# Kernel tuning notes

Measured on AMD Instinct MI355X. Metric: run time of the kernel, lower is better.

Reference implementation:

```python
import jax, jax.numpy as jnp
import numpy as np

G = 2   # FlipGroup order
H = 16  # num_heads
TEMPERATURE = 1.0


def _shared_w(A, B):
    # Z2 regular-representation equivariant linear: block-circulant weight
    # W = [[A, B], [B, A]], shape (dim, dim)
    return jnp.concatenate([
        jnp.concatenate([A, B], axis=1),
        jnp.concatenate([B, A], axis=1),
    ], axis=0)


def setup_inputs() -> dict:
    key = jax.random.key(0)
    ks = jax.random.split(key, 9)
    d = 1024
    dh = d // G
    inp = {"x": jax.random.normal(ks[0], (4, 1024, d), jnp.float32)}
    for i, n in enumerate(["wqA", "wqB", "wkA", "wkB", "wvA", "wvB", "wpA", "wpB"]):
        inp[n] = jax.random.normal(ks[i + 1], (dh, dh), jnp.float32) * 0.02
    return inp


def reference(x, wqA, wqB, wkA, wkB, wvA, wvB, wpA, wpB):
    B, N, C = x.shape
    hd = C // G // H            # per-group-channel head dim
    scale = hd ** -0.5

    q = x @ _shared_w(wqA, wqB).T
    k = x @ _shared_w(wkA, wkB).T
    v = x @ _shared_w(wvA, wvB).T

    def split(t):
        # (B,N,C) -> (B,H,G,N,hd): per-head features split into G group channels
        return t.reshape(B, N, H, G, hd).transpose(0, 2, 3, 1, 4)

    q, k, v = split(q), split(k), split(v)

    # per-channel attention: independent softmax per (head, group-channel)
    attn = jax.nn.softmax(
        jnp.einsum('bhgnd,bhgmd->bhgnm', q, k) * (scale / TEMPERATURE), axis=-1)
    o = jnp.einsum('bhgnm,bhgmd->bhgnd', attn, v)

    o = o.transpose(0, 3, 1, 2, 4).reshape(B, N, C)
    return o @ _shared_w(wpA, wpB).T
```

## Files before the change

### kernel.cpp

```cpp
#include <hip/hip_runtime.h>


typedef unsigned short ushort_t;
typedef __attribute__((ext_vector_type(4))) unsigned short ushort4_t;
typedef __attribute__((ext_vector_type(8))) unsigned short ushort8;
typedef __attribute__((ext_vector_type(8))) __bf16 bf16x8;
typedef __attribute__((ext_vector_type(4))) float f32x4;
typedef __attribute__((ext_vector_type(4))) unsigned int uint4_t;

#define GPTR(p) ((const __attribute__((address_space(1))) void*)(p))
#define LPTR(p) ((__attribute__((address_space(3))) void*)(p))

static __device__ __forceinline__ unsigned short f2b(float f) {
  unsigned int u = __builtin_bit_cast(unsigned int, f);
  unsigned int r = u + 0x7fffu + ((u >> 16) & 1u);
  return (unsigned short)(r >> 16);
}
static __device__ __forceinline__ float b2f(ushort_t h) {
  unsigned int u = ((unsigned int)h) << 16;
  return __builtin_bit_cast(float, u);
}
static __device__ __forceinline__ unsigned int pack_rtna(float a, float b) {
  const unsigned int ua = (__builtin_bit_cast(unsigned int, a) + 0x8000u) >> 16;
  const unsigned int ub = (__builtin_bit_cast(unsigned int, b) + 0x8000u) & 0xFFFF0000u;
  return ub | ua;
}

__global__ __launch_bounds__(256) void prep_k(
    const float* __restrict__ x,
    const float* __restrict__ wqA, const float* __restrict__ wqB,
    const float* __restrict__ wkA, const float* __restrict__ wkB,
    const float* __restrict__ wvA, const float* __restrict__ wvB,
    const float* __restrict__ wpA, const float* __restrict__ wpB,
    ushort_t* __restrict__ xsd, ushort_t* __restrict__ Wsd, float sclq) {
  const int bid = blockIdx.x;
  if (bid < 1024) {
    const int u = bid * 256 + threadIdx.x;
    const int m = u >> 6;
    const int k8 = (u & 63) * 8;
    const float* p1 = x + (size_t)m * 1024 + k8;
    const float* p2 = p1 + 512;
    const f32x4 a0 = *(const f32x4*)p1,  a1 = *(const f32x4*)(p1 + 4);
    const f32x4 b0 = *(const f32x4*)p2,  b1 = *(const f32x4*)(p2 + 4);
    ushort8 vs, vd;
#pragma unroll
    for (int e = 0; e < 4; ++e) {
      vs[e] = f2b(a0[e] + b0[e]); vs[e + 4] = f2b(a1[e] + b1[e]);
      vd[e] = f2b(a0[e] - b0[e]); vd[e + 4] = f2b(a1[e] - b1[e]);
    }
    *(ushort8*)&xsd[(size_t)m * 1024 + k8] = vs;
    *(ushort8*)&xsd[(size_t)m * 1024 + 512 + k8] = vd;
  } else {
    const int u = (bid - 1024) * 256 + threadIdx.x;
    const int hm = u >> 15;
    const int rem = u & 32767;
    const int r = rem >> 6;
    const int c8 = (rem & 63) * 8;
    const int proj = hm >> 1, isD = hm & 1;
    const float* A; const float* B;
    if (proj == 0)      { A = wqA; B = wqB; }
    else if (proj == 1) { A = wkA; B = wkB; }
    else if (proj == 2) { A = wvA; B = wvB; }
    else                { A = wpA; B = wpB; }
    const float scl = 0.5f * (proj == 0 ? sclq : 1.0f);
    const f32x4 a0 = *(const f32x4*)(A + (size_t)r * 512 + c8);
    const f32x4 a1 = *(const f32x4*)(A + (size_t)r * 512 + c8 + 4);
    const f32x4 b0 = *(const f32x4*)(B + (size_t)r * 512 + c8);
    const f32x4 b1 = *(const f32x4*)(B + (size_t)r * 512 + c8 + 4);
    ushort8 v;
#pragma unroll
    for (int e = 0; e < 4; ++e) {
      v[e]     = f2b(isD ? (a0[e] - b0[e]) * scl : (a0[e] + b0[e]) * scl);
      v[e + 4] = f2b(isD ? (a1[e] - b1[e]) * scl : (a1[e] + b1[e]) * scl);
    }
    *(ushort8*)&Wsd[(size_t)(proj * 1024 + isD * 512 + r) * 512 + c8] = v;
  }
}

__global__ __launch_bounds__(256, 3) void gemm_sd_qkv(const ushort_t* __restrict__ xsd,
                                                      const ushort_t* __restrict__ Wsd,
                                                      ushort_t* __restrict__ Qb,
                                                      ushort_t* __restrict__ Kb,
                                                      ushort_t* __restrict__ Vtb) {
  __shared__ ushort_t sh[24576];

  const int t = threadIdx.x;
  const int wid = t >> 6, lane = t & 63;
  const int wm = wid >> 1, half = wid & 1;
  const int lr = lane & 15, lg = lane >> 4;

  const int bid = blockIdx.x;
  const int c = bid & 7, j = bid >> 3;
  const int mt = c * 4 + (j & 3);
  const int nzt = j >> 2;
  const int z = nzt >> 3;
  const int n0 = (nzt & 7) * 64;
  const int m0 = mt * 128;

  f32x4 acc[4][4];
  const f32x4 fz = {0.f, 0.f, 0.f, 0.f};
#pragma unroll
  for (int mf = 0; mf < 4; ++mf)
#pragma unroll
    for (int nf = 0; nf < 4; ++nf) acc[mf][nf] = fz;

#define ISSUE(kt_, s_)                                                                   \
  {                                                                                      \
    ushort_t* base_ = sh + (s_) * 12288;                                                 \
    const int k0_ = (kt_) * 32;                                                          \
    _Pragma("unroll") for (int rnd = 0; rnd < 2; ++rnd) {                                \
      const int ch = rnd * 256 + t;                                                      \
      const int row = ch >> 2, cs = ch & 3;                                              \
      const int gcol = k0_ + ((cs ^ ((row >> 1) & 3)) << 3);                             \
      __builtin_amdgcn_global_load_lds(GPTR(xsd + (size_t)(m0 + row) * 1024 + gcol),     \
                                       LPTR(base_ + (size_t)ch * 8), 16, 0, 0);          \
      __builtin_amdgcn_global_load_lds(GPTR(xsd + (size_t)(m0 + row) * 1024 + 512 + gcol),\
                                       LPTR(base_ + 4096 + (size_t)ch * 8), 16, 0, 0);   \
    }                                                                                    \
    {                                                                                    \
      const int row = t >> 2, cs = t & 3;                                                \
      const int gcol = k0_ + ((cs ^ ((row >> 1) & 3)) << 3);                             \
      __builtin_amdgcn_global_load_lds(                                                  \
          GPTR(Wsd + (size_t)(z * 1024 + n0 + row) * 512 + gcol),                        \
          LPTR(sh + (s_) * 12288 + 8192 + (size_t)t * 8), 16, 0, 0);                     \
      __builtin_amdgcn_global_load_lds(                                                  \
          GPTR(Wsd + (size_t)(z * 1024 + 512 + n0 + row) * 512 + gcol),                  \
          LPTR(sh + (s_) * 12288 + 10240 + (size_t)t * 8), 16, 0, 0);                    \
    }                                                                                    \
  }

  ISSUE(0, 0)
  for (int kt = 0; kt < 16; ++kt) {
    const int s = kt & 1;
    asm volatile("" ::: "memory");
    __builtin_amdgcn_s_barrier();
    asm volatile("" ::: "memory");
    if (kt < 15) {
      ISSUE(kt + 1, s ^ 1)
      asm volatile("s_waitcnt vmcnt(6)" ::: "memory");
    } else {
      asm volatile("s_waitcnt vmcnt(0)" ::: "memory");
    }
    __builtin_amdgcn_sched_barrier(0);
    __builtin_amdgcn_s_barrier();
    asm volatile("" ::: "memory");

    const ushort_t* base = sh + s * 12288;
    const ushort_t* Asl = base + half * 4096;
    const ushort_t* Bsl = base + 8192 + half * 2048;
    bf16x8 a[4], b[4];
#pragma unroll
    for (int mf = 0; mf < 4; ++mf) {
      const int row = wm * 64 + mf * 16 + lr;
      a[mf] = *(const bf16x8*)&Asl[row * 32 + ((lg ^ ((row >> 1) & 3)) << 3)];
    }
#pragma unroll
    for (int nf = 0; nf < 4; ++nf) {
      const int row = nf * 16 + lr;
      b[nf] = *(const bf16x8*)&Bsl[row * 32 + ((lg ^ ((row >> 1) & 3)) << 3)];
    }
    __builtin_amdgcn_s_setprio(1);
#pragma unroll
    for (int mf = 0; mf < 4; ++mf)
#pragma unroll
      for (int nf = 0; nf < 4; ++nf)
        acc[mf][nf] = __builtin_amdgcn_mfma_f32_16x16x32_bf16(a[mf], b[nf], acc[mf][nf], 0, 0, 0);
    __builtin_amdgcn_s_setprio(0);
  }
#undef ISSUE

  __syncthreads();
  const int PAD = (z < 2) ? 72 : 73;
  ushort_t* tus = sh;
  ushort_t* tvd = sh + 128 * PAD;
  {
    ushort_t* dst = half ? tvd : tus;
#pragma unroll
    for (int mf = 0; mf < 4; ++mf)
#pragma unroll
      for (int nf = 0; nf < 4; ++nf)
#pragma unroll
        for (int rr = 0; rr < 4; ++rr) {
          const int row = wm * 64 + mf * 16 + lg * 4 + rr;
          const int col = nf * 16 + lr;
          dst[row * PAD + col] = f2b(acc[mf][nf][rr]);
        }
  }
  __syncthreads();

  if (z < 2) {
    ushort_t* C = (z == 0) ? Qb : Kb;
#pragma unroll
    for (int it = 0; it < 4; ++it) {
      const int idx = it * 256 + t;
      const int row = idx >> 3;
      const int c8 = (idx & 7) * 8;
      const ushort8 u8 = *(const ushort8*)&tus[row * 72 + c8];
      const ushort8 v8 = *(const ushort8*)&tvd[row * 72 + c8];
      ushort8 y1, y2;
#pragma unroll
      for (int e = 0; e < 8; ++e) {
        const float us = b2f(u8[e]), vd = b2f(v8[e]);
        y1[e] = f2b(us + vd);
        y2[e] = f2b(us - vd);
      }
      *(ushort8*)&C[(size_t)(m0 + row) * 1024 + n0 + c8] = y1;
      *(ushort8*)&C[(size_t)(m0 + row) * 1024 + 512 + n0 + c8] = y2;
    }
  } else {
    const int bidx = m0 >> 10, tok0 = m0 & 1023;
#pragma unroll
    for (int it = 0; it < 4; ++it) {
      const int idx = it * 256 + t;
      const int cr = idx >> 4;
      const int mc = (idx & 15) * 8;
      float y1v[8], y2v[8];
#pragma unroll
      for (int e = 0; e < 8; ++e) {
        const float us = b2f(tus[(mc + e) * 73 + cr]);
        const float vd = b2f(tvd[(mc + e) * 73 + cr]);
        y1v[e] = us + vd;
        y2v[e] = us - vd;
      }
      const int k6 = mc & 63;
      const int base = (k6 & 0x20) | ((k6 & 8) << 1) | ((k6 & 0x10) >> 2);
      const size_t rb1 = (size_t)bidx * 1024 * 1024 + (size_t)(n0 + cr) * 1024 +
                         tok0 + (mc & ~63) + base;
      const size_t rb2 = (size_t)bidx * 1024 * 1024 + (size_t)(512 + n0 + cr) * 1024 +
                         tok0 + (mc & ~63) + base;
      ushort4_t lo1, hi1, lo2, hi2;
#pragma unroll
      for (int e = 0; e < 4; ++e) {
        lo1[e] = f2b(y1v[e]); hi1[e] = f2b(y1v[e + 4]);
        lo2[e] = f2b(y2v[e]); hi2[e] = f2b(y2v[e + 4]);
      }
      *(ushort4_t*)&Vtb[rb1] = lo1;  *(ushort4_t*)&Vtb[rb1 + 8] = hi1;
      *(ushort4_t*)&Vtb[rb2] = lo2;  *(ushort4_t*)&Vtb[rb2 + 8] = hi2;
    }
  }
}

__global__ __launch_bounds__(512, 4) void attn_k(const ushort_t* __restrict__ Q,
                                                 const ushort_t* __restrict__ K,
                                                 const ushort_t* __restrict__ Vt,
                                                 ushort_t* __restrict__ Osd) {
  __shared__ ushort_t shmem[32768];
  ushort_t* KsL = shmem;
  ushort_t* VsL = shmem + 16384;
  float* obuf = (float*)shmem;

  const int t = threadIdx.x;
  const int w = t >> 6, lane = t & 63;
  const int hw = w >> 2;
  const int lr = lane & 15, lg = lane >> 4, lk8 = lg * 8;
  const int rkey = (lr >> 1) & 3;
  const int pkey = lr & 7;

  const int nlin = blockIdx.x;
  const int c = nlin & 7, j = nlin >> 3;
  const int p = c * 8 + (j >> 3);
  const int qb = j & 7;
  const int hp = p & 15, b = p >> 4;

  const size_t bbase = (size_t)b * 1024 * 1024;
  const size_t headc = (size_t)hp * 32 + hw * 512;
  const int q0 = qb * 128 + (w & 3) * 32;
  const f32x4 fzero = {0.f, 0.f, 0.f, 0.f};

  bf16x8 bq[2];
#pragma unroll
  for (int i = 0; i < 2; ++i)
    bq[i] = *(const bf16x8*)&Q[bbase + (size_t)(q0 + i * 16 + lr) * 1024 + headc + lk8];

  f32x4 oacc[2][2];
  float tq[2] = {0.f, 0.f};
#pragma unroll
  for (int i = 0; i < 2; ++i)
#pragma unroll
    for (int jj = 0; jj < 2; ++jj) oacc[i][jj] = fzero;

#define ISSUE_KV(kt_, s_)                                                                \
  {                                                                                      \
    ushort_t* Kd_ = KsL + (s_) * 4096;                                                   \
    ushort_t* Vd_ = VsL + (s_) * 4096;                                                   \
    const int hl = t >> 8, rem = t & 255;                                                \
    const size_t hc_ = (size_t)hp * 32 + hl * 512;                                       \
    const int krow = rem >> 2, kc = rem & 3;                                             \
    __builtin_amdgcn_global_load_lds(                                                    \
        GPTR(K + bbase + (size_t)((kt_) * 64 + krow) * 1024 + hc_ +                      \
             ((kc ^ ((krow >> 1) & 3)) << 3)),                                           \
        LPTR(Kd_ + (size_t)t * 8), 16, 0, 0);                                            \
    const int vrow = rem >> 3, vc = rem & 7;                                             \
    __builtin_amdgcn_global_load_lds(                                                    \
        GPTR(Vt + bbase + (size_t)(hc_ + vrow) * 1024 + (kt_) * 64 +                     \
             ((vc ^ (vrow & 7)) << 3)),                                                  \
        LPTR(Vd_ + (size_t)t * 8), 16, 0, 0);                                            \
  }

  ISSUE_KV(0, 0) ISSUE_KV(1, 1) ISSUE_KV(2, 2)
  for (int kt = 0; kt < 16; ++kt) {
    const int s = kt & 3;
    asm volatile("" ::: "memory");
    __builtin_amdgcn_s_barrier();
    asm volatile("" ::: "memory");
    if (kt < 13) {
      ISSUE_KV(kt + 3, (kt + 3) & 3)
      asm volatile("s_waitcnt vmcnt(6)" ::: "memory");
    } else if (kt == 13) {
      asm volatile("s_waitcnt vmcnt(4)" ::: "memory");
    } else if (kt == 14) {
      asm volatile("s_waitcnt vmcnt(2)" ::: "memory");
    } else {
      asm volatile("s_waitcnt vmcnt(0)" ::: "memory");
    }
    __builtin_amdgcn_sched_barrier(0);
    __builtin_amdgcn_s_barrier();
    asm volatile("" ::: "memory");

    const ushort_t* Ksb = KsL + s * 4096 + hw * 2048;
    const ushort_t* Vsb = VsL + s * 4096 + hw * 2048;

    bf16x8 ak[4];
#pragma unroll
    for (int kf = 0; kf < 4; ++kf)
      ak[kf] = *(const bf16x8*)&Ksb[(kf * 16 + lr) * 32 + ((lg ^ rkey) << 3)];

    bf16x8 ap[2][2];
#pragma unroll
    for (int i = 0; i < 2; ++i) {
      f32x4 s4[4];
      __builtin_amdgcn_s_setprio(1);
#pragma unroll
      for (int kf = 0; kf < 4; ++kf)
        s4[kf] = __builtin_amdgcn_mfma_f32_16x16x32_bf16(ak[kf], bq[i], fzero, 0, 0, 0);
      __builtin_amdgcn_s_setprio(0);
#pragma unroll
      for (int ks = 0; ks < 2; ++ks) {
        const float p0 = __builtin_amdgcn_exp2f(s4[2 * ks][0]);
        const float p1 = __builtin_amdgcn_exp2f(s4[2 * ks][1]);
        const float p2 = __builtin_amdgcn_exp2f(s4[2 * ks][2]);
        const float p3 = __builtin_amdgcn_exp2f(s4[2 * ks][3]);
        const float p4 = __builtin_amdgcn_exp2f(s4[2 * ks + 1][0]);
        const float p5 = __builtin_amdgcn_exp2f(s4[2 * ks + 1][1]);
        const float p6 = __builtin_amdgcn_exp2f(s4[2 * ks + 1][2]);
        const float p7 = __builtin_amdgcn_exp2f(s4[2 * ks + 1][3]);
        tq[i] += ((p0 + p1) + (p2 + p3)) + ((p4 + p5) + (p6 + p7));
        uint4_t u;
        u[0] = pack_rtna(p0, p1);
        u[1] = pack_rtna(p2, p3);
        u[2] = pack_rtna(p4, p5);
        u[3] = pack_rtna(p6, p7);
        ap[i][ks] = __builtin_bit_cast(bf16x8, u);
      }
    }

#pragma unroll
    for (int ks = 0; ks < 2; ++ks) {
      bf16x8 bv0 = *(const bf16x8*)&Vsb[(0 * 16 + lr) * 64 + ((ks * 32 + lk8) ^ (pkey << 3))];
      bf16x8 bv1 = *(const bf16x8*)&Vsb[(1 * 16 + lr) * 64 + ((ks * 32 + lk8) ^ (pkey << 3))];
      __builtin_amdgcn_s_setprio(1);
#pragma unroll
      for (int i = 0; i < 2; ++i) {
        oacc[i][0] = __builtin_amdgcn_mfma_f32_16x16x32_bf16(ap[i][ks], bv0, oacc[i][0], 0, 0, 0);
        oacc[i][1] = __builtin_amdgcn_mfma_f32_16x16x32_bf16(ap[i][ks], bv1, oacc[i][1], 0, 0, 0);
      }
      __builtin_amdgcn_s_setprio(0);
    }
  }
#undef ISSUE_KV

#pragma unroll
  for (int i = 0; i < 2; ++i) {
    tq[i] += __shfl_xor(tq[i], 16, 64);
    tq[i] += __shfl_xor(tq[i], 32, 64);
  }

  __syncthreads();
#pragma unroll
  for (int i = 0; i < 2; ++i) {
    float inv[4];
#pragma unroll
    for (int r = 0; r < 4; ++r)
      inv[r] = 1.0f / __shfl(tq[i], lg * 4 + r, 64);
#pragma unroll
    for (int jj = 0; jj < 2; ++jj)
#pragma unroll
      for (int r = 0; r < 4; ++r) {
        const int row = (w & 3) * 32 + i * 16 + lg * 4 + r;
        obuf[hw * 4224 + row * 33 + jj * 16 + lr] = oacc[i][jj][r] * inv[r];
      }
  }
  __syncthreads();

  {
    const int row = t >> 2;
    const int c8 = (t & 3) * 8;
    ushort8 vs, vd;
#pragma unroll
    for (int e = 0; e < 8; ++e) {
      const float o0 = obuf[0 * 4224 + row * 33 + c8 + e];
      const float o1 = obuf[1 * 4224 + row * 33 + c8 + e];
      vs[e] = f2b(o0 + o1);
      vd[e] = f2b(o0 - o1);
    }
    const size_t rowg = bbase + (size_t)(qb * 128 + row) * 1024;
    *(ushort8*)&Osd[rowg + hp * 32 + c8] = vs;
    *(ushort8*)&Osd[rowg + 512 + hp * 32 + c8] = vd;
  }
}

__global__ __launch_bounds__(256, 4) void gemm_out_sd(const ushort_t* __restrict__ Osd,
                                                      const ushort_t* __restrict__ Wsd,
                                                      float* __restrict__ out) {
  __shared__ ushort_t sh[24576];

  const int t = threadIdx.x;
  const int w = t >> 6, lane = t & 63;
  const int wm = w >> 1, half = w & 1;
  const int lr = lane & 15, lg = lane >> 4;

  const int bid = blockIdx.x;
  const int c = bid & 7, j = bid >> 3;
  const int mt = c * 8 + (j & 7);
  const int st = j >> 3;
  const int m0 = mt * 64, n0s = st * 64;

  f32x4 acc[2][4];
  const f32x4 fz = {0.f, 0.f, 0.f, 0.f};
#pragma unroll
  for (int mf = 0; mf < 2; ++mf)
#pragma unroll
    for (int nf = 0; nf < 4; ++nf) acc[mf][nf] = fz;

#define ISSUE_O(kt_, s_)                                                                 \
  {                                                                                      \
    ushort_t* base_ = sh + (s_) * 8192;                                                  \
    const int k0_ = (kt_) * 32;                                                          \
    const int row = t >> 2, kc = t & 3;                                                  \
    const int gcol = k0_ + ((kc ^ ((row >> 1) & 3)) << 3);                               \
    __builtin_amdgcn_global_load_lds(GPTR(Osd + (size_t)(m0 + row) * 1024 + gcol),       \
                                     LPTR(base_ + (size_t)t * 8), 16, 0, 0);             \
    __builtin_amdgcn_global_load_lds(GPTR(Osd + (size_t)(m0 + row) * 1024 + 512 + gcol), \
                                     LPTR(base_ + 2048 + (size_t)t * 8), 16, 0, 0);      \
    __builtin_amdgcn_global_load_lds(                                                    \
        GPTR(Wsd + (size_t)(3072 + n0s + row) * 512 + gcol),                             \
        LPTR(base_ + 4096 + (size_t)t * 8), 16, 0, 0);                                   \
    __builtin_amdgcn_global_load_lds(                                                    \
        GPTR(Wsd + (size_t)(3072 + 512 + n0s + row) * 512 + gcol),                       \
        LPTR(base_ + 6144 + (size_t)t * 8), 16, 0, 0);                                   \
  }

  ISSUE_O(0, 0) ISSUE_O(1, 1)
  int s = 0;
  for (int kt = 0; kt < 16; ++kt) {
    asm volatile("" ::: "memory");
    __builtin_amdgcn_s_barrier();
    asm volatile("" ::: "memory");
    if (kt < 14) {
      const int s2 = (s >= 1) ? s - 1 : 2;
      ISSUE_O(kt + 2, s2)
      asm volatile("s_waitcnt vmcnt(8)" ::: "memory");
    } else if (kt == 14) {
      asm volatile("s_waitcnt vmcnt(4)" ::: "memory");
    } else {
      asm volatile("s_waitcnt vmcnt(0)" ::: "memory");
    }
    __builtin_amdgcn_sched_barrier(0);
    __builtin_amdgcn_s_barrier();
    asm volatile("" ::: "memory");

    const ushort_t* base = sh + s * 8192;
    const ushort_t* Asl = base + half * 2048;
    const ushort_t* Bsl = base + 4096 + half * 2048;
    bf16x8 a[2], b[4];
#pragma unroll
    for (int mf = 0; mf < 2; ++mf) {
      const int row = wm * 32 + mf * 16 + lr;
      a[mf] = *(const bf16x8*)&Asl[row * 32 + ((lg ^ ((row >> 1) & 3)) << 3)];
    }
#pragma unroll
    for (int nf = 0; nf < 4; ++nf) {
      const int row = nf * 16 + lr;
      b[nf] = *(const bf16x8*)&Bsl[row * 32 + ((lg ^ ((row >> 1) & 3)) << 3)];
    }
    __builtin_amdgcn_s_setprio(1);
#pragma unroll
    for (int mf = 0; mf < 2; ++mf)
#pragma unroll
      for (int nf = 0; nf < 4; ++nf)
        acc[mf][nf] = __builtin_amdgcn_mfma_f32_16x16x32_bf16(a[mf], b[nf], acc[mf][nf], 0, 0, 0);
    __builtin_amdgcn_s_setprio(0);
    s = (s == 2) ? 0 : s + 1;
  }
#undef ISSUE_O

  __syncthreads();
  float* vdbuf = (float*)sh;
  if (half == 1) {
#pragma unroll
    for (int mf = 0; mf < 2; ++mf)
#pragma unroll
      for (int nf = 0; nf < 4; ++nf)
#pragma unroll
        for (int rr = 0; rr < 4; ++rr) {
          const int row = wm * 32 + mf * 16 + lg * 4 + rr;
          const int col = nf * 16 + lr;
          vdbuf[row * 66 + col] = acc[mf][nf][rr];
        }
  }
  __syncthreads();
  if (half == 0) {
#pragma unroll
    for (int mf = 0; mf < 2; ++mf)
#pragma unroll
      for (int nf = 0; nf < 4; ++nf)
#pragma unroll
        for (int rr = 0; rr < 4; ++rr) {
          const int row = wm * 32 + mf * 16 + lg * 4 + rr;
          const int col = nf * 16 + lr;
          const float us = acc[mf][nf][rr];
          const float vd = vdbuf[row * 66 + col];
          out[(size_t)(m0 + row) * 1024 + n0s + col] = us + vd;
          out[(size_t)(m0 + row) * 1024 + 512 + n0s + col] = us - vd;
        }
  }
}

extern "C" void kernel_launch(void* const* d_in, const int* in_sizes, int n_in,
                              void* d_out, int out_size, void* d_ws, size_t ws_size,
                              hipStream_t stream) {
  const float* x   = (const float*)d_in[0];
  const float* wqA = (const float*)d_in[1];
  const float* wqB = (const float*)d_in[2];
  const float* wkA = (const float*)d_in[3];
  const float* wkB = (const float*)d_in[4];
  const float* wvA = (const float*)d_in[5];
  const float* wvB = (const float*)d_in[6];
  const float* wpA = (const float*)d_in[7];
  const float* wpB = (const float*)d_in[8];
  float* out = (float*)d_out;

  const size_t NE = (size_t)4096 * 1024;
  ushort_t* Qb   = (ushort_t*)d_ws;
  ushort_t* Kb   = Qb + NE;
  ushort_t* Vtb  = Kb + NE;
  ushort_t* xsd  = Vtb + NE;
  ushort_t* Wsd  = xsd + NE;
  ushort_t* Osd  = xsd;

  const float SCL = 0.17677669529663687f * 1.4426950408889634f;

  prep_k<<<2048, 256, 0, stream>>>(x, wqA, wqB, wkA, wkB, wvA, wvB, wpA, wpB,
                                   xsd, Wsd, SCL);
  gemm_sd_qkv<<<768, 256, 0, stream>>>(xsd, Wsd, Qb, Kb, Vtb);
  attn_k<<<512, 512, 0, stream>>>(Qb, Kb, Vtb, Osd);
  gemm_out_sd<<<512, 256, 0, stream>>>(Osd, Wsd, out);

  (void)in_sizes; (void)n_in; (void)out_size; (void)ws_size;
}
```

Measured before the change: 80.63 us.

## Widen QKV GEMM tile to 128 columns with 512 threads and 4-stage pipeline

The QKV GEMM now uses 512-thread blocks covering a 128x128 output tile (per sum/diff half), halving the grid. The two-stage double buffer is replaced by a four-stage LDS ring with loads issued three steps ahead. The MFMA work is split into two phases with staged X and W loads placed between them. This aims to improve reuse of the x tile and hide global load latency, at the cost of 128 KB of LDS per block, which limits occupancy, and more barriers per k-step.

```diff
diff --git a/kernel.cpp b/kernel.cpp
--- a/kernel.cpp
+++ b/kernel.cpp
@@ -77,25 +77,28 @@
   }
 }
 
-__global__ __launch_bounds__(256, 3) void gemm_sd_qkv(const ushort_t* __restrict__ xsd,
+__global__ __launch_bounds__(512, 2) void gemm_sd_qkv(const ushort_t* __restrict__ xsd,
                                                       const ushort_t* __restrict__ Wsd,
                                                       ushort_t* __restrict__ Qb,
                                                       ushort_t* __restrict__ Kb,
                                                       ushort_t* __restrict__ Vtb) {
-  __shared__ ushort_t sh[24576];
+  __shared__ ushort_t sh[65536];
 
   const int t = threadIdx.x;
   const int wid = t >> 6, lane = t & 63;
-  const int wm = wid >> 1, half = wid & 1;
+  const int wm = wid >> 2, sp = (wid >> 1) & 1, half = wid & 1;
   const int lr = lane & 15, lg = lane >> 4;
 
   const int bid = blockIdx.x;
   const int c = bid & 7, j = bid >> 3;
   const int mt = c * 4 + (j & 3);
-  const int nzt = j >> 2;
-  const int z = nzt >> 3;
-  const int n0 = (nzt & 7) * 64;
+  const int nz = j >> 2;
+  const int z = nz >> 2;
+  const int n0sp = (nz & 3) * 128;
   const int m0 = mt * 128;
+
+  const int srow = t >> 2, scs = t & 3;
+  const int sswz = (scs ^ ((srow >> 1) & 3)) << 3;
 
   f32x4 acc[4][4];
   const f32x4 fz = {0.f, 0.f, 0.f, 0.f};
@@ -104,73 +107,101 @@
 #pragma unroll
     for (int nf = 0; nf < 4; ++nf) acc[mf][nf] = fz;
 
-#define ISSUE(kt_, s_)                                                                   \
+#define STAGE_X(kt_, s_)                                                                 \
   {                                                                                      \
-    ushort_t* base_ = sh + (s_) * 12288;                                                 \
-    const int k0_ = (kt_) * 32;                                                          \
-    _Pragma("unroll") for (int rnd = 0; rnd < 2; ++rnd) {                                \
-      const int ch = rnd * 256 + t;                                                      \
-      const int row = ch >> 2, cs = ch & 3;                                              \
-      const int gcol = k0_ + ((cs ^ ((row >> 1) & 3)) << 3);                             \
-      __builtin_amdgcn_global_load_lds(GPTR(xsd + (size_t)(m0 + row) * 1024 + gcol),     \
-                                       LPTR(base_ + (size_t)ch * 8), 16, 0, 0);          \
-      __builtin_amdgcn_global_load_lds(GPTR(xsd + (size_t)(m0 + row) * 1024 + 512 + gcol),\
-                                       LPTR(base_ + 4096 + (size_t)ch * 8), 16, 0, 0);   \
-    }                                                                                    \
-    {                                                                                    \
-      const int row = t >> 2, cs = t & 3;                                                \
-      const int gcol = k0_ + ((cs ^ ((row >> 1) & 3)) << 3);                             \
-      __builtin_amdgcn_global_load_lds(                                                  \
-          GPTR(Wsd + (size_t)(z * 1024 + n0 + row) * 512 + gcol),                        \
-          LPTR(sh + (s_) * 12288 + 8192 + (size_t)t * 8), 16, 0, 0);                     \
-      __builtin_amdgcn_global_load_lds(                                                  \
-          GPTR(Wsd + (size_t)(z * 1024 + 512 + n0 + row) * 512 + gcol),                  \
-          LPTR(sh + (s_) * 12288 + 10240 + (size_t)t * 8), 16, 0, 0);                    \
-    }                                                                                    \
-  }
-
-  ISSUE(0, 0)
+    ushort_t* b_ = sh + (s_) * 16384;                                                    \
+    const int gcol = (kt_) * 32 + sswz;                                                  \
+    __builtin_amdgcn_global_load_lds(GPTR(xsd + (size_t)(m0 + srow) * 1024 + gcol),      \
+                                     LPTR(b_ + (size_t)t * 8), 16, 0, 0);                \
+    __builtin_amdgcn_global_load_lds(GPTR(xsd + (size_t)(m0 + srow) * 1024 + 512 + gcol),\
+                                     LPTR(b_ + 4096 + (size_t)t * 8), 16, 0, 0);         \
+  }
+#define STAGE_W(kt_, s_)                                                                 \
+  {                                                                                      \
+    ushort_t* b_ = sh + (s_) * 16384;                                                    \
+    const int gcol = (kt_) * 32 + sswz;                                                  \
+    __builtin_amdgcn_global_load_lds(                                                    \
+        GPTR(Wsd + (size_t)(z * 1024 + n0sp + srow) * 512 + gcol),                       \
+        LPTR(b_ + 8192 + (size_t)t * 8), 16, 0, 0);                                      \
+    __builtin_amdgcn_global_load_lds(                                                    \
+        GPTR(Wsd + (size_t)(z * 1024 + 512 + n0sp + srow) * 512 + gcol),                 \
+        LPTR(b_ + 12288 + (size_t)t * 8), 16, 0, 0);                                     \
+  }
+
+  STAGE_X(0, 0) STAGE_W(0, 0)
+  STAGE_X(1, 1) STAGE_W(1, 1)
+  STAGE_X(2, 2) STAGE_W(2, 2)
+  asm volatile("s_waitcnt vmcnt(8)" ::: "memory");
+  __builtin_amdgcn_sched_barrier(0);
+  __builtin_amdgcn_s_barrier();
+  asm volatile("" ::: "memory");
+
   for (int kt = 0; kt < 16; ++kt) {
-    const int s = kt & 1;
-    asm volatile("" ::: "memory");
-    __builtin_amdgcn_s_barrier();
-    asm volatile("" ::: "memory");
-    if (kt < 15) {
-      ISSUE(kt + 1, s ^ 1)
-      asm volatile("s_waitcnt vmcnt(6)" ::: "memory");
-    } else {
+    const int s = kt & 3;
+    const ushort_t* base = sh + s * 16384;
+    const ushort_t* Asl = base + half * 4096;
+    const ushort_t* Bsl = base + 8192 + half * 4096;
+
+    bf16x8 a0, a1, b[4];
+    {
+      const int r0 = wm * 64 + 0 * 16 + lr;
+      const int r1 = wm * 64 + 1 * 16 + lr;
+      a0 = *(const bf16x8*)&Asl[r0 * 32 + ((lg ^ ((r0 >> 1) & 3)) << 3)];
+      a1 = *(const bf16x8*)&Asl[r1 * 32 + ((lg ^ ((r1 >> 1) & 3)) << 3)];
+#pragma unroll
+      for (int nf = 0; nf < 4; ++nf) {
+        const int rb = sp * 64 + nf * 16 + lr;
+        b[nf] = *(const bf16x8*)&Bsl[rb * 32 + ((lg ^ ((rb >> 1) & 3)) << 3)];
+      }
+    }
+    if (kt <= 12) STAGE_X(kt + 3, (kt + 3) & 3)
+    __builtin_amdgcn_s_barrier();
+    asm volatile("s_waitcnt lgkmcnt(0)" ::: "memory");
+    __builtin_amdgcn_sched_barrier(0);
+    __builtin_amdgcn_s_setprio(1);
+#pragma unroll
+    for (int nf = 0; nf < 4; ++nf) {
+      acc[0][nf] = __builtin_amdgcn_mfma_f32_16x16x32_bf16(a0, b[nf], acc[0][nf], 0, 0, 0);
+      acc[1][nf] = __builtin_amdgcn_mfma_f32_16x16x32_bf16(a1, b[nf], acc[1][nf], 0, 0, 0);
+    }
+    __builtin_amdgcn_s_setprio(0);
+    __builtin_amdgcn_s_barrier();
+    asm volatile("" ::: "memory");
+
+    bf16x8 a2, a3;
+    {
+      const int r2 = wm * 64 + 2 * 16 + lr;
+      const int r3 = wm * 64 + 3 * 16 + lr;
+      a2 = *(const bf16x8*)&Asl[r2 * 32 + ((lg ^ ((r2 >> 1) & 3)) << 3)];
+      a3 = *(const bf16x8*)&Asl[r3 * 32 + ((lg ^ ((r3 >> 1) & 3)) << 3)];
+    }
+    if (kt <= 12) STAGE_W(kt + 3, (kt + 3) & 3)
+    if (kt <= 12) {
+      asm volatile("s_waitcnt vmcnt(8)" ::: "memory");
+    } else if (kt == 13) {
+      asm volatile("s_waitcnt vmcnt(4)" ::: "memory");
+    } else if (kt == 14) {
       asm volatile("s_waitcnt vmcnt(0)" ::: "memory");
     }
     __builtin_amdgcn_sched_barrier(0);
     __builtin_amdgcn_s_barrier();
-    asm volatile("" ::: "memory");
-
-    const ushort_t* base = sh + s * 12288;
-    const ushort_t* Asl = base + half * 4096;
-    const ushort_t* Bsl = base + 8192 + half * 2048;
-    bf16x8 a[4], b[4];
-#pragma unroll
-    for (int mf = 0; mf < 4; ++mf) {
-      const int row = wm * 64 + mf * 16 + lr;
-      a[mf] = *(const bf16x8*)&Asl[row * 32 + ((lg ^ ((row >> 1) & 3)) << 3)];
-    }
+    asm volatile("s_waitcnt lgkmcnt(0)" ::: "memory");
+    __builtin_amdgcn_sched_barrier(0);
+    __builtin_amdgcn_s_setprio(1);
 #pragma unroll
     for (int nf = 0; nf < 4; ++nf) {
-      const int row = nf * 16 + lr;
-      b[nf] = *(const bf16x8*)&Bsl[row * 32 + ((lg ^ ((row >> 1) & 3)) << 3)];
-    }
-    __builtin_amdgcn_s_setprio(1);
-#pragma unroll
-    for (int mf = 0; mf < 4; ++mf)
-#pragma unroll
-      for (int nf = 0; nf < 4; ++nf)
-        acc[mf][nf] = __builtin_amdgcn_mfma_f32_16x16x32_bf16(a[mf], b[nf], acc[mf][nf], 0, 0, 0);
+      acc[2][nf] = __builtin_amdgcn_mfma_f32_16x16x32_bf16(a2, b[nf], acc[2][nf], 0, 0, 0);
+      acc[3][nf] = __builtin_amdgcn_mfma_f32_16x16x32_bf16(a3, b[nf], acc[3][nf], 0, 0, 0);
+    }
     __builtin_amdgcn_s_setprio(0);
-  }
-#undef ISSUE
+    __builtin_amdgcn_s_barrier();
+    asm volatile("" ::: "memory");
+  }
+#undef STAGE_X
+#undef STAGE_W
 
   __syncthreads();
-  const int PAD = (z < 2) ? 72 : 73;
+  const int PAD = (z < 2) ? 136 : 137;
   ushort_t* tus = sh;
   ushort_t* tvd = sh + 128 * PAD;
   {
@@ -182,7 +213,7 @@
 #pragma unroll
         for (int rr = 0; rr < 4; ++rr) {
           const int row = wm * 64 + mf * 16 + lg * 4 + rr;
-          const int col = nf * 16 + lr;
+          const int col = sp * 64 + nf * 16 + lr;
           dst[row * PAD + col] = f2b(acc[mf][nf][rr]);
         }
   }
@@ -192,11 +223,11 @@
     ushort_t* C = (z == 0) ? Qb : Kb;
 #pragma unroll
     for (int it = 0; it < 4; ++it) {
-      const int idx = it * 256 + t;
-      const int row = idx >> 3;
-      const int c8 = (idx & 7) * 8;
-      const ushort8 u8 = *(const ushort8*)&tus[row * 72 + c8];
-      const ushort8 v8 = *(const ushort8*)&tvd[row * 72 + c8];
+      const int idx = it * 512 + t;
+      const int row = idx >> 4;
+      const int c8 = (idx & 15) * 8;
+      const ushort8 u8 = *(const ushort8*)&tus[row * 136 + c8];
+      const ushort8 v8 = *(const ushort8*)&tvd[row * 136 + c8];
       ushort8 y1, y2;
 #pragma unroll
       for (int e = 0; e < 8; ++e) {
@@ -204,29 +235,29 @@
         y1[e] = f2b(us + vd);
         y2[e] = f2b(us - vd);
       }
-      *(ushort8*)&C[(size_t)(m0 + row) * 1024 + n0 + c8] = y1;
-      *(ushort8*)&C[(size_t)(m0 + row) * 1024 + 512 + n0 + c8] = y2;
+      *(ushort8*)&C[(size_t)(m0 + row) * 1024 + n0sp + c8] = y1;
+      *(ushort8*)&C[(size_t)(m0 + row) * 1024 + 512 + n0sp + c8] = y2;
     }
   } else {
     const int bidx = m0 >> 10, tok0 = m0 & 1023;
 #pragma unroll
     for (int it = 0; it < 4; ++it) {
-      const int idx = it * 256 + t;
+      const int idx = it * 512 + t;
       const int cr = idx >> 4;
       const int mc = (idx & 15) * 8;
       float y1v[8], y2v[8];
 #pragma unroll
       for (int e = 0; e < 8; ++e) {
-        const float us = b2f(tus[(mc + e) * 73 + cr]);
-        const float vd = b2f(tvd[(mc + e) * 73 + cr]);
+        const float us = b2f(tus[(mc + e) * 137 + cr]);
+        const float vd = b2f(tvd[(mc + e) * 137 + cr]);
         y1v[e] = us + vd;
         y2v[e] = us - vd;
       }
       const int k6 = mc & 63;
       const int base = (k6 & 0x20) | ((k6 & 8) << 1) | ((k6 & 0x10) >> 2);
-      const size_t rb1 = (size_t)bidx * 1024 * 1024 + (size_t)(n0 + cr) * 1024 +
+      const size_t rb1 = (size_t)bidx * 1024 * 1024 + (size_t)(n0sp + cr) * 1024 +
                          tok0 + (mc & ~63) + base;
-      const size_t rb2 = (size_t)bidx * 1024 * 1024 + (size_t)(512 + n0 + cr) * 1024 +
+      const size_t rb2 = (size_t)bidx * 1024 * 1024 + (size_t)(512 + n0sp + cr) * 1024 +
                          tok0 + (mc & ~63) + base;
       ushort4_t lo1, hi1, lo2, hi2;
 #pragma unroll
@@ -552,7 +583,7 @@
 
   prep_k<<<2048, 256, 0, stream>>>(x, wqA, wqB, wkA, wkB, wvA, wvB, wpA, wpB,
                                    xsd, Wsd, SCL);
-  gemm_sd_qkv<<<768, 256, 0, stream>>>(xsd, Wsd, Qb, Kb, Vtb);
+  gemm_sd_qkv<<<384, 512, 0, stream>>>(xsd, Wsd, Qb, Kb, Vtb);
   attn_k<<<512, 512, 0, stream>>>(Qb, Kb, Vtb, Osd);
   gemm_out_sd<<<512, 256, 0, stream>>>(Osd, Wsd, out);
 
```

Result: slower. 84.73 us (+5.1%).
